# Kernel optimization log

Hardware: AMD Instinct MI355X
Metric: run time of the kernel (lower is better)

Reference implementation:

```python
import jax, jax.numpy as jnp
import numpy as np

D = 1024
H = 16
HD = D // H
SCALE = HD ** -0.5


def setup_inputs() -> dict:
    key = jax.random.key(0)
    ks = jax.random.split(key, 5)
    x = jax.random.normal(ks[0], (2, 2048, D), dtype=jnp.float32)
    s = 1.0 / np.sqrt(D)
    W_qkv = jax.random.uniform(ks[1], (D, 3 * D), jnp.float32, -s, s)
    b_qkv = jax.random.uniform(ks[2], (3 * D,), jnp.float32, -s, s)
    W_out = jax.random.uniform(ks[3], (D, D), jnp.float32, -s, s)
    b_out = jax.random.uniform(ks[4], (D,), jnp.float32, -s, s)
    return {"x": x, "W_qkv": W_qkv, "b_qkv": b_qkv, "W_out": W_out, "b_out": b_out}


def reference(x, W_qkv, b_qkv, W_out, b_out):
    B, S, _ = x.shape
    qkv = x @ W_qkv + b_qkv                       # [B,S,3D]
    qkv = qkv.reshape(B, S, 3, H, HD)
    q, k, v = jnp.moveaxis(qkv, 2, 0)             # each [B,S,H,HD]
    # scores: [B,H,S,S]
    scores = jnp.einsum("bshd,bthd->bhst", q, k) * SCALE
    attn = jax.nn.softmax(scores, axis=-1)        # dropout is identity in eval mode
    out = jnp.einsum("bhst,bthd->bshd", attn, v)  # [B,S,H,HD]
    out = out.reshape(B, S, H * HD)
    return out @ W_out + b_out
```

## Files before the change

kernel.cpp:

```cpp
#include <hip/hip_runtime.h>

typedef unsigned short u16;
typedef unsigned int   u32;

using short8 = __attribute__((ext_vector_type(8))) short;
using f32x4  = __attribute__((ext_vector_type(4))) float;
using half4  = __attribute__((ext_vector_type(4))) _Float16;

#define QSCALE 0.18033688011112042f

__device__ __forceinline__ u16 f2bf(float f) {
  u32 u = __float_as_uint(f);
  return (u16)((u + 0x8000u) >> 16);
}
__device__ __forceinline__ u16 f2h(float f) {
  _Float16 h = (_Float16)f;
  return __builtin_bit_cast(u16, h);
}

__device__ __forceinline__ void gld16(const u16* g, u16* l) {
  __builtin_amdgcn_global_load_lds(
      (const __attribute__((address_space(1))) unsigned int*)g,
      (__attribute__((address_space(3))) unsigned int*)l, 16, 0, 0);
}

__global__ __launch_bounds__(256) void cvt_x(const float* __restrict__ in,
                                             u16* __restrict__ out) {
  int idx = blockIdx.x * 256 + threadIdx.x;
  float4 v = reinterpret_cast<const float4*>(in)[idx];
  ushort4 o;
  o.x = f2bf(v.x); o.y = f2bf(v.y); o.z = f2bf(v.z); o.w = f2bf(v.w);
  reinterpret_cast<ushort4*>(out)[idx] = o;
}

__global__ __launch_bounds__(256) void transpose_w(const float* __restrict__ in,
                                                   u16* __restrict__ out,
                                                   int R, int C) {
  __shared__ u32 s[32][33];
  int c0 = blockIdx.x * 32, r0 = blockIdx.y * 32;
  int j = threadIdx.x & 31, i0 = threadIdx.x >> 5;
#pragma unroll
  for (int p = 0; p < 4; ++p) {
    int i = i0 + p * 8;
    s[i][j] = f2bf(in[(size_t)(r0 + i) * C + c0 + j]);
  }
  __syncthreads();
#pragma unroll
  for (int p = 0; p < 4; ++p) {
    int jj = i0 + p * 8;
    out[(size_t)(c0 + jj) * R + r0 + j] = (u16)s[j][jj];
  }
}

template <int EPI, int MT>
__global__ __launch_bounds__(256, 2) void gemm_bt(
    const u16* __restrict__ A, const u16* __restrict__ Bt,
    const float* __restrict__ bias, float* __restrict__ c_out,
    u16* __restrict__ q_out, u16* __restrict__ k_out, u16* __restrict__ vt_out,
    int M, int N, int K) {
  __shared__ __align__(16) u16 As[32 * MT * 32];
  __shared__ __align__(16) u16 Bs[128 * 32];
  const int tid = threadIdx.x;
  const int lane = tid & 63;
  const int wv = tid >> 6;
  const int l16 = lane & 15, quad = lane >> 4;
  const int wm = wv & 1, wn = wv >> 1;
  const int bx = blockIdx.x, by = blockIdx.y;

  const u16* Ab = A + (size_t)by * (32 * MT) * K;
  const u16* Bb = Bt + (size_t)bx * 128 * K;

  const f32x4 fzero = {0.0f, 0.0f, 0.0f, 0.0f};
  f32x4 acc[MT][4];
#pragma unroll
  for (int i = 0; i < MT; ++i)
#pragma unroll
    for (int j = 0; j < 4; ++j) acc[i][j] = fzero;

  for (int k0 = 0; k0 < K; k0 += 32) {
    __syncthreads();
#pragma unroll
    for (int p = 0; p < MT / 2; ++p) {
      int id = p * 256 + tid;
      int row = id >> 2, blk = id & 3;
      int gc = k0 + ((blk ^ (row & 3)) << 3);
      gld16(Ab + (size_t)row * K + gc, &As[id << 3]);
    }
#pragma unroll
    for (int p = 0; p < 2; ++p) {
      int id = p * 256 + tid;
      int row = id >> 2, blk = id & 3;
      int gc = k0 + ((blk ^ (row & 3)) << 3);
      gld16(Bb + (size_t)row * K + gc, &Bs[id << 3]);
    }
    __syncthreads();
    short8 af[MT], bfr[4];
#pragma unroll
    for (int mi = 0; mi < MT; ++mi) {
      int row = wm * (MT * 16) + mi * 16 + l16;
      af[mi] = *reinterpret_cast<const short8*>(&As[row * 32 + ((quad ^ (row & 3)) << 3)]);
    }
#pragma unroll
    for (int ni = 0; ni < 4; ++ni) {
      int row = wn * 64 + ni * 16 + l16;
      bfr[ni] = *reinterpret_cast<const short8*>(&Bs[row * 32 + ((quad ^ (row & 3)) << 3)]);
    }
#pragma unroll
    for (int mi = 0; mi < MT; ++mi)
#pragma unroll
      for (int ni = 0; ni < 4; ++ni)
        acc[mi][ni] = __builtin_amdgcn_mfma_f32_16x16x32_bf16(af[mi], bfr[ni], acc[mi][ni], 0, 0, 0);
  }

#pragma unroll
  for (int mi = 0; mi < MT; ++mi)
#pragma unroll
    for (int ni = 0; ni < 4; ++ni) {
      int col = bx * 128 + wn * 64 + ni * 16 + l16;
      float bv = bias[col];
      int row0 = by * (32 * MT) + wm * (MT * 16) + mi * 16 + quad * 4;
      if (EPI == 1) {
#pragma unroll
        for (int r = 0; r < 4; ++r)
          c_out[(size_t)(row0 + r) * N + col] = acc[mi][ni][r] + bv;
      } else {
        int which = col >> 10, rem = col & 1023;
        int h = rem >> 6, d = rem & 63;
        int b = row0 >> 11, sq0 = row0 & 2047;
        int bh = (b << 4) + h;
        if (which == 2) {
          ushort4 pk;
          pk.x = f2h(acc[mi][ni][0] + bv);
          pk.y = f2h(acc[mi][ni][1] + bv);
          pk.z = f2h(acc[mi][ni][2] + bv);
          pk.w = f2h(acc[mi][ni][3] + bv);
          *reinterpret_cast<ushort4*>(&vt_out[(size_t)bh * 131072 + d * 2048 + sq0]) = pk;
        } else {
          size_t base = (size_t)(bh * 2048 + sq0) * 64 + d;
#pragma unroll
          for (int r = 0; r < 4; ++r) {
            float val = acc[mi][ni][r] + bv;
            if (which == 0) q_out[base + r * 64] = f2bf(val * QSCALE);
            else            k_out[base + r * 64] = f2bf(val);
          }
        }
      }
    }
}

__global__ __launch_bounds__(256, 4) void attn(
    const u16* __restrict__ q_buf, const u16* __restrict__ k_buf,
    const u16* __restrict__ vt_buf, u16* __restrict__ o_buf) {
  __shared__ __align__(16) u16 Qs[64 * 64];
  __shared__ __align__(16) u16 Ks[2][64 * 64];
  __shared__ __align__(16) u16 Vts[2][64 * 64];

  const int tid = threadIdx.x;
  const int lane = tid & 63, w = tid >> 6;
  const int l16 = lane & 15, quad = lane >> 4;
  const int bh = blockIdx.y, q0 = blockIdx.x * 64;

  const u16* qg = q_buf + (size_t)bh * 131072 + q0 * 64;
  const u16* kg = k_buf + (size_t)bh * 131072;
  const u16* vg = vt_buf + (size_t)bh * 131072;

#pragma unroll
  for (int p = 0; p < 2; ++p) {
    int id = p * 256 + tid;
    int row = id >> 3, blk = id & 7;
    int so = (blk ^ (row & 7)) << 3;
    gld16(qg + row * 64 + so, &Qs[id << 3]);
    gld16(kg + row * 64 + so, &Ks[0][id << 3]);
    gld16(vg + row * 2048 + so, &Vts[0][id << 3]);
  }

  const f32x4 fzero = {0.0f, 0.0f, 0.0f, 0.0f};
  f32x4 o_acc[4];
  f32x4 o_l = fzero;
#pragma unroll
  for (int nd = 0; nd < 4; ++nd) o_acc[nd] = fzero;
  half4 ones;
#pragma unroll
  for (int j = 0; j < 4; ++j) ones[j] = (_Float16)1.0f;

  __syncthreads();

  const int qrow = w * 16 + l16;
  short8 qb[2];
#pragma unroll
  for (int kk = 0; kk < 2; ++kk)
    qb[kk] = *reinterpret_cast<const short8*>(
        &Qs[qrow * 64 + (((kk * 4 + quad) ^ (qrow & 7)) << 3)]);

  for (int i = 0; i < 32; ++i) {
    const int buf = i & 1;
    if (i + 1 < 32) {
      const int nxt = buf ^ 1;
      const int t1 = (i + 1) * 64;
#pragma unroll
      for (int p = 0; p < 2; ++p) {
        int id = p * 256 + tid;
        int row = id >> 3, blk = id & 7;
        int so = (blk ^ (row & 7)) << 3;
        gld16(kg + (t1 + row) * 64 + so, &Ks[nxt][id << 3]);
        gld16(vg + row * 2048 + t1 + so, &Vts[nxt][id << 3]);
      }
    }

    f32x4 s[4];
#pragma unroll
    for (int ti = 0; ti < 4; ++ti) s[ti] = fzero;
#pragma unroll
    for (int kk = 0; kk < 2; ++kk)
#pragma unroll
      for (int ti = 0; ti < 4; ++ti) {
        int kr = ti * 16 + l16;
        short8 ka = *reinterpret_cast<const short8*>(
            &Ks[buf][kr * 64 + (((kk * 4 + quad) ^ (kr & 7)) << 3)]);
        s[ti] = __builtin_amdgcn_mfma_f32_16x16x32_bf16(ka, qb[kk], s[ti], 0, 0, 0);
      }

#pragma unroll
    for (int ti = 0; ti < 4; ++ti) {
      half4 pa;
#pragma unroll
      for (int j = 0; j < 4; ++j)
        pa[j] = (_Float16)__builtin_amdgcn_exp2f(s[ti][j]);
      o_l = __builtin_amdgcn_mfma_f32_16x16x16f16(pa, ones, o_l, 0, 0, 0);
#pragma unroll
      for (int nd = 0; nd < 4; ++nd) {
        int d = nd * 16 + l16;
        int tloc = ti * 16 + quad * 4;
        const half4 vb = *reinterpret_cast<const half4*>(
            &Vts[buf][d * 64 + ((((tloc >> 3) ^ (d & 7)) << 3) | (tloc & 7))]);
        o_acc[nd] = __builtin_amdgcn_mfma_f32_16x16x16f16(pa, vb, o_acc[nd], 0, 0, 0);
      }
    }

    __syncthreads();
  }

  const int b = bh >> 4, h = bh & 15;
#pragma unroll
  for (int r = 0; r < 4; ++r) {
    int sq = q0 + w * 16 + quad * 4 + r;
    float inv = 1.0f / o_l[r];
    size_t base = (size_t)(b * 2048 + sq) * 1024 + h * 64;
#pragma unroll
    for (int nd = 0; nd < 4; ++nd)
      o_buf[base + nd * 16 + l16] = f2bf(o_acc[nd][r] * inv);
  }
}

extern "C" void kernel_launch(void* const* d_in, const int* in_sizes, int n_in,
                              void* d_out, int out_size, void* d_ws, size_t ws_size,
                              hipStream_t stream) {
  (void)in_sizes; (void)n_in; (void)out_size; (void)ws_size;
  const float* x     = (const float*)d_in[0];
  const float* W_qkv = (const float*)d_in[1];
  const float* b_qkv = (const float*)d_in[2];
  const float* W_out = (const float*)d_in[3];
  const float* b_out = (const float*)d_in[4];
  float* out = (float*)d_out;

  char* ws = (char*)d_ws;
  u16* x_bf   = (u16*)(ws);
  u16* wqkv_t = (u16*)(ws + 8388608);
  u16* wout_t = (u16*)(ws + 14680064);
  u16* q_buf  = (u16*)(ws + 16777216);
  u16* k_buf  = (u16*)(ws + 25165824);
  u16* vt_buf = (u16*)(ws + 33554432);
  u16* o_bf   = (u16*)(ws + 41943040);

  cvt_x<<<4096, 256, 0, stream>>>(x, x_bf);
  transpose_w<<<dim3(96, 32), 256, 0, stream>>>(W_qkv, wqkv_t, 1024, 3072);
  transpose_w<<<dim3(32, 32), 256, 0, stream>>>(W_out, wout_t, 1024, 1024);
  gemm_bt<0, 4><<<dim3(24, 32), 256, 0, stream>>>(x_bf, wqkv_t, b_qkv, nullptr,
                                                  q_buf, k_buf, vt_buf, 4096, 3072, 1024);
  attn<<<dim3(32, 32), 256, 0, stream>>>(q_buf, k_buf, vt_buf, o_bf);
  gemm_bt<1, 2><<<dim3(8, 64), 256, 0, stream>>>(o_bf, wout_t, b_out, out,
                                                 nullptr, nullptr, nullptr, 4096, 1024, 1024);
}
```

Measured before the change: 194.0 us.

## Split attention keys across waves and tile-swizzle V^T layout from QKV GEMM

The attention kernel now has each wave own 16 key rows of each 64-key tile for all 64 queries, instead of 16 queries against all keys. Q fragments are held in registers and loaded straight from global memory. Partial outputs and row sums are reduced across waves through shared memory at the end, and row sums are built with scalar adds instead of an extra MFMA against ones. The QKV GEMM epilogue writes V^T in a per-64-token tiled, XOR-swizzled layout so each tile can be copied into LDS contiguously. Occupancy hints change to 3 for both kernels, and the new layout adds a cross-wave reduction step plus more accumulator registers.

Result: slower. 198.4 us (+2.3%).

```diff
diff --git a/kernel.cpp b/kernel.cpp
--- a/kernel.cpp
+++ b/kernel.cpp
@@ -53,7 +53,7 @@
 }
 
 template <int EPI, int MT>
-__global__ __launch_bounds__(256, 2) void gemm_bt(
+__global__ __launch_bounds__(256, 3) void gemm_bt(
     const u16* __restrict__ A, const u16* __restrict__ Bt,
     const float* __restrict__ bias, float* __restrict__ c_out,
     u16* __restrict__ q_out, u16* __restrict__ k_out, u16* __restrict__ vt_out,
@@ -129,12 +129,15 @@
         int b = row0 >> 11, sq0 = row0 & 2047;
         int bh = (b << 4) + h;
         if (which == 2) {
+          int tile = sq0 >> 6;
+          int sub = ((sq0 >> 2) & 15) ^ (d & 15);
           ushort4 pk;
           pk.x = f2h(acc[mi][ni][0] + bv);
           pk.y = f2h(acc[mi][ni][1] + bv);
           pk.z = f2h(acc[mi][ni][2] + bv);
           pk.w = f2h(acc[mi][ni][3] + bv);
-          *reinterpret_cast<ushort4*>(&vt_out[(size_t)bh * 131072 + d * 2048 + sq0]) = pk;
+          *reinterpret_cast<ushort4*>(
+              &vt_out[(size_t)bh * 131072 + tile * 4096 + d * 64 + (sub << 2)]) = pk;
         } else {
           size_t base = (size_t)(bh * 2048 + sq0) * 64 + d;
 #pragma unroll
@@ -148,12 +151,11 @@
     }
 }
 
-__global__ __launch_bounds__(256, 4) void attn(
+__global__ __launch_bounds__(256, 3) void attn(
     const u16* __restrict__ q_buf, const u16* __restrict__ k_buf,
     const u16* __restrict__ vt_buf, u16* __restrict__ o_buf) {
-  __shared__ __align__(16) u16 Qs[64 * 64];
-  __shared__ __align__(16) u16 Ks[2][64 * 64];
-  __shared__ __align__(16) u16 Vts[2][64 * 64];
+  __shared__ __align__(16) u16 smem[2][2][4096];
+  __shared__ __align__(16) float lred[256];
 
   const int tid = threadIdx.x;
   const int lane = tid & 63, w = tid >> 6;
@@ -164,91 +166,137 @@
   const u16* kg = k_buf + (size_t)bh * 131072;
   const u16* vg = vt_buf + (size_t)bh * 131072;
 
+  short8 qb[4][2];
+#pragma unroll
+  for (int qi = 0; qi < 4; ++qi)
+#pragma unroll
+    for (int kk = 0; kk < 2; ++kk)
+      qb[qi][kk] = *reinterpret_cast<const short8*>(
+          qg + (qi * 16 + l16) * 64 + kk * 32 + quad * 8);
+
 #pragma unroll
   for (int p = 0; p < 2; ++p) {
     int id = p * 256 + tid;
     int row = id >> 3, blk = id & 7;
-    int so = (blk ^ (row & 7)) << 3;
-    gld16(qg + row * 64 + so, &Qs[id << 3]);
-    gld16(kg + row * 64 + so, &Ks[0][id << 3]);
-    gld16(vg + row * 2048 + so, &Vts[0][id << 3]);
+    gld16(kg + row * 64 + ((blk ^ (row & 7)) << 3), &smem[0][0][id << 3]);
+    gld16(vg + id * 8, &smem[0][1][id << 3]);
   }
 
   const f32x4 fzero = {0.0f, 0.0f, 0.0f, 0.0f};
-  f32x4 o_acc[4];
-  f32x4 o_l = fzero;
-#pragma unroll
-  for (int nd = 0; nd < 4; ++nd) o_acc[nd] = fzero;
-  half4 ones;
-#pragma unroll
-  for (int j = 0; j < 4; ++j) ones[j] = (_Float16)1.0f;
+  f32x4 o_acc[4][4];
+  float l_acc[4] = {0.f, 0.f, 0.f, 0.f};
+#pragma unroll
+  for (int qi = 0; qi < 4; ++qi)
+#pragma unroll
+    for (int nd = 0; nd < 4; ++nd) o_acc[qi][nd] = fzero;
+
+  const int kr = w * 16 + l16;
+  const int ka_off0 = kr * 64 + (((0 * 4 + quad) ^ (kr & 7)) << 3);
+  const int ka_off1 = kr * 64 + (((1 * 4 + quad) ^ (kr & 7)) << 3);
+  const int vb_off = l16 * 64 + ((((w * 4 + quad) ^ l16)) << 2);
 
   __syncthreads();
-
-  const int qrow = w * 16 + l16;
-  short8 qb[2];
-#pragma unroll
-  for (int kk = 0; kk < 2; ++kk)
-    qb[kk] = *reinterpret_cast<const short8*>(
-        &Qs[qrow * 64 + (((kk * 4 + quad) ^ (qrow & 7)) << 3)]);
 
   for (int i = 0; i < 32; ++i) {
     const int buf = i & 1;
     if (i + 1 < 32) {
       const int nxt = buf ^ 1;
-      const int t1 = (i + 1) * 64;
 #pragma unroll
       for (int p = 0; p < 2; ++p) {
         int id = p * 256 + tid;
         int row = id >> 3, blk = id & 7;
-        int so = (blk ^ (row & 7)) << 3;
-        gld16(kg + (t1 + row) * 64 + so, &Ks[nxt][id << 3]);
-        gld16(vg + row * 2048 + t1 + so, &Vts[nxt][id << 3]);
+        gld16(kg + ((i + 1) * 64 + row) * 64 + ((blk ^ (row & 7)) << 3),
+              &smem[nxt][0][id << 3]);
+        gld16(vg + (i + 1) * 4096 + id * 8, &smem[nxt][1][id << 3]);
       }
     }
 
     f32x4 s[4];
 #pragma unroll
-    for (int ti = 0; ti < 4; ++ti) s[ti] = fzero;
-#pragma unroll
-    for (int kk = 0; kk < 2; ++kk)
-#pragma unroll
-      for (int ti = 0; ti < 4; ++ti) {
-        int kr = ti * 16 + l16;
-        short8 ka = *reinterpret_cast<const short8*>(
-            &Ks[buf][kr * 64 + (((kk * 4 + quad) ^ (kr & 7)) << 3)]);
-        s[ti] = __builtin_amdgcn_mfma_f32_16x16x32_bf16(ka, qb[kk], s[ti], 0, 0, 0);
-      }
-
-#pragma unroll
-    for (int ti = 0; ti < 4; ++ti) {
-      half4 pa;
-#pragma unroll
-      for (int j = 0; j < 4; ++j)
-        pa[j] = (_Float16)__builtin_amdgcn_exp2f(s[ti][j]);
-      o_l = __builtin_amdgcn_mfma_f32_16x16x16f16(pa, ones, o_l, 0, 0, 0);
+    for (int qi = 0; qi < 4; ++qi) s[qi] = fzero;
+    {
+      short8 ka0 = *reinterpret_cast<const short8*>(&smem[buf][0][ka_off0]);
+      short8 ka1 = *reinterpret_cast<const short8*>(&smem[buf][0][ka_off1]);
+#pragma unroll
+      for (int qi = 0; qi < 4; ++qi) {
+        s[qi] = __builtin_amdgcn_mfma_f32_16x16x32_bf16(ka0, qb[qi][0], s[qi], 0, 0, 0);
+        s[qi] = __builtin_amdgcn_mfma_f32_16x16x32_bf16(ka1, qb[qi][1], s[qi], 0, 0, 0);
+      }
+    }
+
+    half4 pa[4];
+#pragma unroll
+    for (int qi = 0; qi < 4; ++qi) {
+      float p0 = __builtin_amdgcn_exp2f(s[qi][0]);
+      float p1 = __builtin_amdgcn_exp2f(s[qi][1]);
+      float p2 = __builtin_amdgcn_exp2f(s[qi][2]);
+      float p3 = __builtin_amdgcn_exp2f(s[qi][3]);
+      l_acc[qi] += (p0 + p1) + (p2 + p3);
+      pa[qi][0] = (_Float16)p0; pa[qi][1] = (_Float16)p1;
+      pa[qi][2] = (_Float16)p2; pa[qi][3] = (_Float16)p3;
+    }
+
+#pragma unroll
+    for (int nd = 0; nd < 4; ++nd) {
+      half4 vb = *reinterpret_cast<const half4*>(&smem[buf][1][vb_off + nd * 1024]);
+#pragma unroll
+      for (int qi = 0; qi < 4; ++qi)
+        o_acc[qi][nd] = __builtin_amdgcn_mfma_f32_16x16x16f16(pa[qi], vb, o_acc[qi][nd], 0, 0, 0);
+    }
+
+    __syncthreads();
+  }
+
+#pragma unroll
+  for (int qi = 0; qi < 4; ++qi) {
+    l_acc[qi] += __shfl_xor(l_acc[qi], 16, 64);
+    l_acc[qi] += __shfl_xor(l_acc[qi], 32, 64);
+  }
+  if (lane < 16) {
+#pragma unroll
+    for (int qi = 0; qi < 4; ++qi) lred[(w * 4 + qi) * 16 + lane] = l_acc[qi];
+  }
+
+  float* fb = (float*)smem;
+  const int b = bh >> 4, h = bh & 15;
+
+#pragma unroll
+  for (int phase = 0; phase < 2; ++phase) {
+#pragma unroll
+    for (int qq = 0; qq < 2; ++qq) {
+      int qi = phase * 2 + qq;
+#pragma unroll
+      for (int nd = 0; nd < 4; ++nd)
+        *reinterpret_cast<f32x4*>(&fb[((w * 2 + qq) * 4 + nd) * 256 + lane * 4]) =
+            o_acc[qi][nd];
+    }
+    __syncthreads();
+    if ((w >> 1) == phase) {
+      const int sel = w & 1;
+      f32x4 lv = fzero;
+#pragma unroll
+      for (int wp = 0; wp < 4; ++wp)
+        lv += *reinterpret_cast<const f32x4*>(&lred[(wp * 4 + w) * 16 + quad * 4]);
+      f32x4 os[4];
 #pragma unroll
       for (int nd = 0; nd < 4; ++nd) {
-        int d = nd * 16 + l16;
-        int tloc = ti * 16 + quad * 4;
-        const half4 vb = *reinterpret_cast<const half4*>(
-            &Vts[buf][d * 64 + ((((tloc >> 3) ^ (d & 7)) << 3) | (tloc & 7))]);
-        o_acc[nd] = __builtin_amdgcn_mfma_f32_16x16x16f16(pa, vb, o_acc[nd], 0, 0, 0);
-      }
-    }
-
-    __syncthreads();
-  }
-
-  const int b = bh >> 4, h = bh & 15;
-#pragma unroll
-  for (int r = 0; r < 4; ++r) {
-    int sq = q0 + w * 16 + quad * 4 + r;
-    float inv = 1.0f / o_l[r];
-    size_t base = (size_t)(b * 2048 + sq) * 1024 + h * 64;
-#pragma unroll
-    for (int nd = 0; nd < 4; ++nd)
-      o_buf[base + nd * 16 + l16] = f2bf(o_acc[nd][r] * inv);
+        os[nd] = fzero;
+#pragma unroll
+        for (int wp = 0; wp < 4; ++wp)
+          os[nd] += *reinterpret_cast<const f32x4*>(
+              &fb[((wp * 2 + sel) * 4 + nd) * 256 + lane * 4]);
+      }
+#pragma unroll
+      for (int r = 0; r < 4; ++r) {
+        int sq = q0 + w * 16 + quad * 4 + r;
+        float inv = 1.0f / lv[r];
+        size_t base = (size_t)(b * 2048 + sq) * 1024 + h * 64;
+#pragma unroll
+        for (int nd = 0; nd < 4; ++nd)
+          o_buf[base + nd * 16 + l16] = f2bf(os[nd][r] * inv);
+      }
+    }
+    __syncthreads();
   }
 }
 
```
